# Kernel optimization log

Hardware: AMD Instinct MI355X
Metric: run time of the kernel (lower is better)

The kernel has to match this reference:

```python
import jax, jax.numpy as jnp
import numpy as np

DIM = 768
N_HEADS = 12
HEAD_DIM = DIM // N_HEADS
HIDDEN = int(DIM * 4.0)
B, S = 4, 2048
EPS = 1e-6
SCALE = HEAD_DIM ** -0.5


def layer_norm(x, gamma, beta):
    mu = jnp.mean(x, axis=-1, keepdims=True)
    var = jnp.mean((x - mu) ** 2, axis=-1, keepdims=True)
    return (x - mu) * jax.lax.rsqrt(var + EPS) * gamma + beta


def setup_inputs() -> dict:
    key = jax.random.key(0)
    ks = jax.random.split(key, 8)
    x = jax.random.normal(ks[0], (B, S, DIM), dtype=jnp.float32)
    mask = jax.random.randint(ks[1], (B, 1, S, S), 0, 2, dtype=jnp.int32)
    sd = DIM ** -0.5
    return {
        "x": x,
        "mask": mask,
        "w_qkv": jax.random.normal(ks[2], (DIM, 3 * DIM), dtype=jnp.float32) * sd,
        "b_qkv": jnp.zeros((3 * DIM,), jnp.float32),
        "w_proj": jax.random.normal(ks[3], (DIM, DIM), dtype=jnp.float32) * sd,
        "b_proj": jnp.zeros((DIM,), jnp.float32),
        "g1": jnp.ones((DIM,), jnp.float32),
        "beta1": jnp.zeros((DIM,), jnp.float32),
        "g2": jnp.ones((DIM,), jnp.float32),
        "beta2": jnp.zeros((DIM,), jnp.float32),
        "w1": jax.random.normal(ks[4], (DIM, HIDDEN), dtype=jnp.float32) * sd,
        "b1": jnp.zeros((HIDDEN,), jnp.float32),
        "w2": jax.random.normal(ks[5], (HIDDEN, DIM), dtype=jnp.float32) * (HIDDEN ** -0.5),
        "b2": jnp.zeros((DIM,), jnp.float32),
    }


def reference(x, mask, w_qkv, b_qkv, w_proj, b_proj, g1, beta1, g2, beta2, w1, b1, w2, b2):
    # --- attention branch (pre-LN) ---
    h = layer_norm(x, g1, beta1)
    qkv = h @ w_qkv + b_qkv                              # (B,S,3*DIM)
    qkv = qkv.reshape(B, S, 3, N_HEADS, HEAD_DIM)
    q, k, v = (qkv[:, :, 0], qkv[:, :, 1], qkv[:, :, 2])  # (B,S,H,D)
    # scores: (B,H,S,S) -- materialized like the original
    dp = jnp.einsum("bqhd,bkhd->bhqk", q, k) * SCALE
    dp = jnp.where(mask == 0, jnp.float32(-10000.0), dp)
    attn = jax.nn.softmax(dp, axis=-1)
    wa = jnp.einsum("bhqk,bkhd->bqhd", attn, v).reshape(B, S, DIM)
    x = x + (wa @ w_proj + b_proj)
    # --- MLP branch (pre-LN) ---
    h = layer_norm(x, g2, beta2)
    h = jax.nn.gelu(h @ w1 + b1, approximate=False)
    x = x + (h @ w2 + b2)
    return x
```

## Files before the change

kernel.cpp:

```cpp
#include <hip/hip_runtime.h>
#include <hip/hip_bf16.h>
#include <math.h>

typedef __bf16 bf16;
typedef __bf16 bf16x8 __attribute__((ext_vector_type(8)));
typedef short bf16x4s __attribute__((ext_vector_type(4)));
typedef float f32x4 __attribute__((ext_vector_type(4)));

#define DIM 768
#define NH 12
#define HD 64
#define HID 3072
#define BB 4
#define SS 2048
#define QPRESCALE 0.18033688011112042f

#define MFMA(a, b, c) __builtin_amdgcn_mfma_f32_16x16x32_bf16(a, b, c, 0, 0, 0)
#define MFMA16(a, b, c) \
  __builtin_amdgcn_mfma_f32_16x16x16bf16_1k(a, b, c, 0, 0, 0)

__device__ __forceinline__ void gld16(const void* g, void* l) {
  __builtin_amdgcn_global_load_lds(
      (const __attribute__((address_space(1))) void*)g,
      (__attribute__((address_space(3))) void*)l, 16, 0, 0);
}

__device__ __forceinline__ unsigned pk2(float a, float b) {
  union {
    bf16 h[2];
    unsigned u;
  } t;
  t.h[0] = (bf16)a;
  t.h[1] = (bf16)b;
  return t.u;
}

__global__ __launch_bounds__(256) void castT_all_kernel(
    const float* __restrict__ s0, bf16* __restrict__ d0,
    const float* __restrict__ s1, bf16* __restrict__ d1,
    const float* __restrict__ s2, bf16* __restrict__ d2,
    const float* __restrict__ s3, bf16* __restrict__ d3) {
  __shared__ float tile[32][33];
  int id = blockIdx.x;
  const float* in;
  bf16* out;
  int R, C, loc;
  if (id < 1728) { in = s0; out = d0; R = 768; C = 2304; loc = id; }
  else if (id < 2304) { in = s1; out = d1; R = 768; C = 768; loc = id - 1728; }
  else if (id < 4608) { in = s2; out = d2; R = 768; C = 3072; loc = id - 2304; }
  else { in = s3; out = d3; R = 3072; C = 768; loc = id - 4608; }
  const int cb = C >> 5;
  const int c0 = (loc % cb) * 32, r0 = (loc / cb) * 32;
  const int tx = threadIdx.x & 31, ty = threadIdx.x >> 5;
#pragma unroll
  for (int i = 0; i < 32; i += 8)
    tile[ty + i][tx] = in[(size_t)(r0 + ty + i) * C + c0 + tx];
  __syncthreads();
#pragma unroll
  for (int i = 0; i < 32; i += 8)
    out[(size_t)(c0 + ty + i) * R + r0 + tx] = (bf16)tile[tx][ty + i];
}

__global__ __launch_bounds__(256) void maskbits_kernel(
    const int* __restrict__ mask, unsigned* __restrict__ bits) {
  const int i = blockIdx.x * 256 + threadIdx.x;
  unsigned long long m = __ballot(mask[i] != 0);
  const int lane = threadIdx.x & 63;
  if (lane == 0) bits[i >> 5] = (unsigned)m;
  else if (lane == 32) bits[i >> 5] = (unsigned)(m >> 32);
}

__global__ __launch_bounds__(256) void ln_kernel(
    const float* __restrict__ x, const float* __restrict__ g,
    const float* __restrict__ beta, bf16* __restrict__ out) {
  const int row = blockIdx.x, t = threadIdx.x;
  const float* xr = x + (size_t)row * DIM;
  float v0 = xr[t], v1 = xr[t + 256], v2 = xr[t + 512];
  float s = v0 + v1 + v2;
  float s2 = v0 * v0 + v1 * v1 + v2 * v2;
#pragma unroll
  for (int d = 1; d < 64; d <<= 1) {
    s += __shfl_xor(s, d);
    s2 += __shfl_xor(s2, d);
  }
  __shared__ float red[8];
  const int wv = t >> 6, lane = t & 63;
  if (lane == 0) { red[wv] = s; red[wv + 4] = s2; }
  __syncthreads();
  s = red[0] + red[1] + red[2] + red[3];
  s2 = red[4] + red[5] + red[6] + red[7];
  const float mu = s * (1.0f / DIM);
  const float var = s2 * (1.0f / DIM) - mu * mu;
  const float r = rsqrtf(var + 1e-6f);
  bf16* o = out + (size_t)row * DIM;
  o[t] = (bf16)((v0 - mu) * r * g[t] + beta[t]);
  o[t + 256] = (bf16)((v1 - mu) * r * g[t + 256] + beta[t + 256]);
  o[t + 512] = (bf16)((v2 - mu) * r * g[t + 512] + beta[t + 512]);
}

enum { EPI_QKV = 0, EPI_PROJ = 1, EPI_FFN1 = 2, EPI_FFN2 = 3 };

template <int EPI, int K, int TN>
__global__ __launch_bounds__(256) void gemm_kernel(
    const bf16* __restrict__ A, const bf16* __restrict__ Bt,
    const float* __restrict__ bias, const float* __restrict__ res,
    void* __restrict__ o0, void* __restrict__ o1, void* __restrict__ o2) {
  constexpr int MI = (TN == 128) ? 4 : 2;
  __shared__ bf16 As[128 * 64];
  __shared__ bf16 Bs[TN * 64];
  const int tid = threadIdx.x;
  const int wv = tid >> 6, lane = tid & 63;
  const int quad = lane >> 4, l15 = lane & 15;
  const int lrow = lane >> 3, lcol = lane & 7;
  const int m0 = blockIdx.y * 128, n0 = blockIdx.x * TN;
  const int wm = (TN == 128) ? (wv >> 1) * 64 : wv * 32;
  const int wn = (TN == 128) ? (wv & 1) * 64 : 0;

  f32x4 acc[MI][4] = {};

  const int swz = (lcol ^ lrow) * 8;
  const bf16* Ag = A + (size_t)(m0 + wv * 32 + lrow) * K + swz;
  const bf16* Bg = Bt + (size_t)(n0 + wv * (TN / 4) + lrow) * K + swz;
  bf16* Al = As + (wv * 32) * 64;
  bf16* Bl = Bs + (wv * (TN / 4)) * 64;

  for (int k0 = 0; k0 < K; k0 += 64) {
#pragma unroll
    for (int i = 0; i < 4; i++)
      gld16(Ag + (size_t)(i * 8) * K + k0, Al + i * 8 * 64);
#pragma unroll
    for (int i = 0; i < TN / 32; i++)
      gld16(Bg + (size_t)(i * 8) * K + k0, Bl + i * 8 * 64);
    __syncthreads();
#pragma unroll
    for (int ks = 0; ks < 2; ks++) {
      bf16x8 af[MI], bfr[4];
#pragma unroll
      for (int i = 0; i < MI; i++) {
        const int ra = wm + i * 16 + l15;
        af[i] = *(const bf16x8*)&As[ra * 64 + ((ks * 4 + quad) ^ (ra & 7)) * 8];
      }
#pragma unroll
      for (int i = 0; i < 4; i++) {
        const int rb = wn + i * 16 + l15;
        bfr[i] = *(const bf16x8*)&Bs[rb * 64 + ((ks * 4 + quad) ^ (rb & 7)) * 8];
      }
#pragma unroll
      for (int mi = 0; mi < MI; mi++)
#pragma unroll
        for (int ni = 0; ni < 4; ni++)
          acc[mi][ni] = MFMA(af[mi], bfr[ni], acc[mi][ni]);
    }
    __syncthreads();
  }

#pragma unroll
  for (int mi = 0; mi < MI; mi++) {
#pragma unroll
    for (int ni = 0; ni < 4; ni++) {
      const int n = n0 + wn + ni * 16 + l15;
      const float bv = bias[n];
      const int mb = m0 + wm + mi * 16 + quad * 4;
      float val[4];
#pragma unroll
      for (int r = 0; r < 4; r++) val[r] = acc[mi][ni][r] + bv;
      if (EPI == EPI_QKV) {
        const int which = n / 768;
        const int nn = n - which * 768;
        const int hh = nn >> 6, d = nn & 63;
        const int bb = mb >> 11, s = mb & 2047;
        if (which == 0) {
#pragma unroll
          for (int r = 0; r < 4; r++)
            ((bf16*)o0)[((size_t)(bb * NH + hh) * SS + s + r) * HD + d] =
                (bf16)(val[r] * QPRESCALE);
        } else if (which == 1) {
#pragma unroll
          for (int r = 0; r < 4; r++)
            ((bf16*)o1)[((size_t)(bb * NH + hh) * SS + s + r) * HD + d] =
                (bf16)val[r];
        } else {
          uint2 pv;
          pv.x = pk2(val[0], val[1]);
          pv.y = pk2(val[2], val[3]);
          *(uint2*)&((bf16*)o2)[((size_t)(bb * NH + hh) * HD + d) * SS + s] = pv;
        }
      } else if (EPI == EPI_PROJ) {
#pragma unroll
        for (int r = 0; r < 4; r++)
          ((float*)o0)[(size_t)(mb + r) * DIM + n] =
              res[(size_t)(mb + r) * DIM + n] + val[r];
      } else if (EPI == EPI_FFN1) {
#pragma unroll
        for (int r = 0; r < 4; r++) {
          const float ge =
              0.5f * val[r] * (1.0f + erff(val[r] * 0.70710678118654752f));
          ((bf16*)o0)[(size_t)(mb + r) * HID + n] = (bf16)ge;
        }
      } else {
#pragma unroll
        for (int r = 0; r < 4; r++)
          ((float*)o0)[(size_t)(mb + r) * DIM + n] =
              res[(size_t)(mb + r) * DIM + n] + val[r];
      }
    }
  }
}

__global__ __launch_bounds__(256) void attn_kernel(
    const bf16* __restrict__ q, const bf16* __restrict__ k,
    const bf16* __restrict__ vT, const unsigned* __restrict__ bits,
    bf16* __restrict__ wa) {
  const int b = blockIdx.z, h = blockIdx.y, q0 = blockIdx.x * 64;
  const int tid = threadIdx.x, wv = tid >> 6, lane = tid & 63;
  const int quad = lane >> 4, l15 = lane & 15;
  const int lrow = lane >> 3, lcol = lane & 7;

  __shared__ bf16 Ks[64 * 64];
  __shared__ bf16 Vs[64 * 64];
  __shared__ unsigned lut[32];

  if (tid < 16) {
    lut[2 * tid] =
        ((tid & 1) ? 0xFFFFu : 0u) | ((tid & 2) ? 0xFFFF0000u : 0u);
    lut[2 * tid + 1] =
        ((tid & 4) ? 0xFFFFu : 0u) | ((tid & 8) ? 0xFFFF0000u : 0u);
  }

  const bf16* qbh = q + (size_t)(b * NH + h) * SS * HD;
  const bf16* kbh = k + (size_t)(b * NH + h) * SS * HD;
  const bf16* vbh = vT + (size_t)(b * NH + h) * HD * SS;

  const int sq = q0 + wv * 16 + l15;
  bf16x8 aq[2];
#pragma unroll
  for (int ks = 0; ks < 2; ks++)
    aq[ks] = *(const bf16x8*)&qbh[(size_t)sq * HD + ks * 32 + quad * 8];

  const unsigned long long* mrow =
      (const unsigned long long*)bits + (size_t)(b * SS + sq) * 32;

  f32x4 O[4] = {};
  f32x4 lm = {};
  const short oneb = 0x3F80;
  const bf16x4s onesA = {oneb, oneb, oneb, oneb};
  const int swz = (lcol ^ lrow) * 8;

  for (int s0 = 0; s0 < SS; s0 += 64) {
#pragma unroll
    for (int i = 0; i < 2; i++) {
      const int r = wv * 16 + i * 8 + lrow;
      gld16(&kbh[(size_t)(s0 + r) * HD + swz], &Ks[(wv * 16 + i * 8) * 64]);
      gld16(&vbh[(size_t)r * SS + s0 + swz], &Vs[(wv * 16 + i * 8) * 64]);
    }
    const unsigned long long sh = mrow[s0 >> 6] >> (quad * 4);
    const unsigned lo32 = (unsigned)sh, hi32 = (unsigned)(sh >> 32);
    __syncthreads();

#pragma unroll
    for (int ni = 0; ni < 4; ni++) {
      const int rr = ni * 16 + l15;
      const bf16x8 kf0 =
          *(const bf16x8*)&Ks[rr * 64 + (quad ^ (rr & 7)) * 8];
      const bf16x8 kf1 =
          *(const bf16x8*)&Ks[rr * 64 + ((4 + quad) ^ (rr & 7)) * 8];
      f32x4 a = {};
      a = MFMA(kf0, aq[0], a);
      a = MFMA(kf1, aq[1], a);
      const unsigned nib = (ni == 0)   ? (lo32 & 0xF)
                           : (ni == 1) ? ((lo32 >> 16) & 0xF)
                           : (ni == 2) ? (hi32 & 0xF)
                                       : ((hi32 >> 16) & 0xF);
      const uint2 mw = *(const uint2*)&lut[2 * nib];
      union {
        unsigned u[2];
        bf16x4s v;
      } pp;
      pp.u[0] = pk2(__builtin_amdgcn_exp2f(a[0]),
                    __builtin_amdgcn_exp2f(a[1])) & mw.x;
      pp.u[1] = pk2(__builtin_amdgcn_exp2f(a[2]),
                    __builtin_amdgcn_exp2f(a[3])) & mw.y;
      lm = MFMA16(onesA, pp.v, lm);
#pragma unroll
      for (int nd = 0; nd < 4; nd++) {
        const int row = nd * 16 + l15;
        const int pc = (ni * 2 + (quad >> 1)) ^ (row & 7);
        const bf16x4s vf =
            *(const bf16x4s*)&Vs[row * 64 + pc * 8 + (quad & 1) * 4];
        O[nd] = MFMA16(vf, pp.v, O[nd]);
      }
    }
    __syncthreads();
  }

  const float rln = __builtin_amdgcn_rcpf(lm[0]);
  bf16* dst = wa + (size_t)(b * SS + sq) * DIM + h * HD + quad * 4;
#pragma unroll
  for (int nd = 0; nd < 4; nd++) {
    uint2 pv;
    pv.x = pk2(O[nd][0] * rln, O[nd][1] * rln);
    pv.y = pk2(O[nd][2] * rln, O[nd][3] * rln);
    *(uint2*)&dst[nd * 16] = pv;
  }
}

extern "C" void kernel_launch(void* const* d_in, const int* in_sizes, int n_in,
                              void* d_out, int out_size, void* d_ws,
                              size_t ws_size, hipStream_t stream) {
  const float* x = (const float*)d_in[0];
  const int* mask = (const int*)d_in[1];
  const float* w_qkv = (const float*)d_in[2];
  const float* b_qkv = (const float*)d_in[3];
  const float* w_proj = (const float*)d_in[4];
  const float* b_proj = (const float*)d_in[5];
  const float* g1 = (const float*)d_in[6];
  const float* beta1 = (const float*)d_in[7];
  const float* g2 = (const float*)d_in[8];
  const float* beta2 = (const float*)d_in[9];
  const float* w1 = (const float*)d_in[10];
  const float* b1 = (const float*)d_in[11];
  const float* w2 = (const float*)d_in[12];
  const float* b2 = (const float*)d_in[13];
  float* out = (float*)d_out;

  char* p = (char*)d_ws;
  auto alloc = [&](size_t bytes) {
    char* r = p;
    p += (bytes + 1023) & ~(size_t)1023;
    return r;
  };
  bf16* wqkvT = (bf16*)alloc((size_t)2304 * 768 * 2);
  bf16* wprojT = (bf16*)alloc((size_t)768 * 768 * 2);
  bf16* w1T = (bf16*)alloc((size_t)3072 * 768 * 2);
  bf16* w2T = (bf16*)alloc((size_t)768 * 3072 * 2);
  unsigned* bits = (unsigned*)alloc((size_t)BB * SS * 64 * 4);
  bf16* h = (bf16*)alloc((size_t)8192 * 768 * 2);
  bf16* qb = (bf16*)alloc((size_t)8192 * 768 * 2);
  bf16* kb = (bf16*)alloc((size_t)8192 * 768 * 2);
  bf16* vtb = (bf16*)alloc((size_t)8192 * 768 * 2);
  bf16* wab = (bf16*)alloc((size_t)8192 * 768 * 2);
  float* x2 = (float*)alloc((size_t)8192 * 768 * 4);
  bf16* ffn1 = (bf16*)alloc((size_t)8192 * 3072 * 2);

  castT_all_kernel<<<6912, 256, 0, stream>>>(w_qkv, wqkvT, w_proj, wprojT, w1,
                                             w1T, w2, w2T);
  maskbits_kernel<<<(BB * SS * SS) / 256, 256, 0, stream>>>(mask, bits);
  ln_kernel<<<8192, 256, 0, stream>>>(x, g1, beta1, h);
  gemm_kernel<EPI_QKV, 768, 128>
      <<<dim3(2304 / 128, 8192 / 128), 256, 0, stream>>>(h, wqkvT, b_qkv,
                                                         nullptr, qb, kb, vtb);
  attn_kernel<<<dim3(SS / 64, NH, BB), 256, 0, stream>>>(qb, kb, vtb, bits,
                                                         wab);
  gemm_kernel<EPI_PROJ, 768, 64>
      <<<dim3(768 / 64, 8192 / 128), 256, 0, stream>>>(wab, wprojT, b_proj, x,
                                                       x2, nullptr, nullptr);
  ln_kernel<<<8192, 256, 0, stream>>>(x2, g2, beta2, h);
  gemm_kernel<EPI_FFN1, 768, 128>
      <<<dim3(3072 / 128, 8192 / 128), 256, 0, stream>>>(h, w1T, b1, nullptr,
                                                         ffn1, nullptr,
                                                         nullptr);
  gemm_kernel<EPI_FFN2, 3072, 64>
      <<<dim3(768 / 64, 8192 / 128), 256, 0, stream>>>(ffn1, w2T, b2, x2, out,
                                                       nullptr, nullptr);
}
```

Baseline: 495.2 us.

## Double-buffer LDS tiles in GEMM and attention kernels to overlap loads

Both the GEMM kernel and the attention kernel now use two LDS buffers. The next K/V or A/B tile is issued via global_load_lds while the current tile is consumed, and the mask word is prefetched one iteration ahead. This keeps one barrier per iteration instead of two and aims to hide global-load latency behind MFMA work. The cost is doubled shared memory, which may reduce occupancy. Correctness relies on the compiler's vmcnt wait before the barrier, since the async LDS loads are only fenced by __syncthreads.

```diff
diff --git a/kernel.cpp b/kernel.cpp
--- a/kernel.cpp
+++ b/kernel.cpp
@@ -106,8 +106,9 @@
     const float* __restrict__ bias, const float* __restrict__ res,
     void* __restrict__ o0, void* __restrict__ o1, void* __restrict__ o2) {
   constexpr int MI = (TN == 128) ? 4 : 2;
-  __shared__ bf16 As[128 * 64];
-  __shared__ bf16 Bs[TN * 64];
+  constexpr int NIT = K / 64;
+  __shared__ bf16 As[2][128 * 64];
+  __shared__ bf16 Bs[2][TN * 64];
   const int tid = threadIdx.x;
   const int wv = tid >> 6, lane = tid & 63;
   const int quad = lane >> 4, l15 = lane & 15;
@@ -121,29 +122,37 @@
   const int swz = (lcol ^ lrow) * 8;
   const bf16* Ag = A + (size_t)(m0 + wv * 32 + lrow) * K + swz;
   const bf16* Bg = Bt + (size_t)(n0 + wv * (TN / 4) + lrow) * K + swz;
-  bf16* Al = As + (wv * 32) * 64;
-  bf16* Bl = Bs + (wv * (TN / 4)) * 64;
-
-  for (int k0 = 0; k0 < K; k0 += 64) {
+
+  auto stage = [&](int buf, int k0) {
 #pragma unroll
     for (int i = 0; i < 4; i++)
-      gld16(Ag + (size_t)(i * 8) * K + k0, Al + i * 8 * 64);
+      gld16(Ag + (size_t)(i * 8) * K + k0, &As[buf][(wv * 32 + i * 8) * 64]);
 #pragma unroll
     for (int i = 0; i < TN / 32; i++)
-      gld16(Bg + (size_t)(i * 8) * K + k0, Bl + i * 8 * 64);
+      gld16(Bg + (size_t)(i * 8) * K + k0,
+            &Bs[buf][(wv * (TN / 4) + i * 8) * 64]);
+  };
+
+  stage(0, 0);
+
+  for (int it = 0; it < NIT; ++it) {
     __syncthreads();
+    if (it + 1 < NIT) stage((it + 1) & 1, (it + 1) * 64);
+    const bf16* Ab = As[it & 1];
+    const bf16* Bb = Bs[it & 1];
 #pragma unroll
     for (int ks = 0; ks < 2; ks++) {
       bf16x8 af[MI], bfr[4];
 #pragma unroll
       for (int i = 0; i < MI; i++) {
         const int ra = wm + i * 16 + l15;
-        af[i] = *(const bf16x8*)&As[ra * 64 + ((ks * 4 + quad) ^ (ra & 7)) * 8];
+        af[i] = *(const bf16x8*)&Ab[ra * 64 + ((ks * 4 + quad) ^ (ra & 7)) * 8];
       }
 #pragma unroll
       for (int i = 0; i < 4; i++) {
         const int rb = wn + i * 16 + l15;
-        bfr[i] = *(const bf16x8*)&Bs[rb * 64 + ((ks * 4 + quad) ^ (rb & 7)) * 8];
+        bfr[i] =
+            *(const bf16x8*)&Bb[rb * 64 + ((ks * 4 + quad) ^ (rb & 7)) * 8];
       }
 #pragma unroll
       for (int mi = 0; mi < MI; mi++)
@@ -151,7 +160,6 @@
         for (int ni = 0; ni < 4; ni++)
           acc[mi][ni] = MFMA(af[mi], bfr[ni], acc[mi][ni]);
     }
-    __syncthreads();
   }
 
 #pragma unroll
@@ -216,8 +224,8 @@
   const int quad = lane >> 4, l15 = lane & 15;
   const int lrow = lane >> 3, lcol = lane & 7;
 
-  __shared__ bf16 Ks[64 * 64];
-  __shared__ bf16 Vs[64 * 64];
+  __shared__ bf16 Ks[2][64 * 64];
+  __shared__ bf16 Vs[2][64 * 64];
   __shared__ unsigned lut[32];
 
   if (tid < 16) {
@@ -246,24 +254,38 @@
   const bf16x4s onesA = {oneb, oneb, oneb, oneb};
   const int swz = (lcol ^ lrow) * 8;
 
-  for (int s0 = 0; s0 < SS; s0 += 64) {
+  auto stageKV = [&](int buf, int s0) {
 #pragma unroll
     for (int i = 0; i < 2; i++) {
       const int r = wv * 16 + i * 8 + lrow;
-      gld16(&kbh[(size_t)(s0 + r) * HD + swz], &Ks[(wv * 16 + i * 8) * 64]);
-      gld16(&vbh[(size_t)r * SS + s0 + swz], &Vs[(wv * 16 + i * 8) * 64]);
-    }
-    const unsigned long long sh = mrow[s0 >> 6] >> (quad * 4);
+      gld16(&kbh[(size_t)(s0 + r) * HD + swz],
+            &Ks[buf][(wv * 16 + i * 8) * 64]);
+      gld16(&vbh[(size_t)r * SS + s0 + swz],
+            &Vs[buf][(wv * 16 + i * 8) * 64]);
+    }
+  };
+
+  stageKV(0, 0);
+  unsigned long long mw = mrow[0];
+
+  for (int t = 0; t < SS / 64; ++t) {
+    __syncthreads();
+    unsigned long long mwn = 0;
+    if (t + 1 < SS / 64) {
+      stageKV((t + 1) & 1, (t + 1) * 64);
+      mwn = mrow[t + 1];
+    }
+    const bf16* Kc = Ks[t & 1];
+    const bf16* Vc = Vs[t & 1];
+    const unsigned long long sh = mw >> (quad * 4);
     const unsigned lo32 = (unsigned)sh, hi32 = (unsigned)(sh >> 32);
-    __syncthreads();
 
 #pragma unroll
     for (int ni = 0; ni < 4; ni++) {
       const int rr = ni * 16 + l15;
-      const bf16x8 kf0 =
-          *(const bf16x8*)&Ks[rr * 64 + (quad ^ (rr & 7)) * 8];
+      const bf16x8 kf0 = *(const bf16x8*)&Kc[rr * 64 + (quad ^ (rr & 7)) * 8];
       const bf16x8 kf1 =
-          *(const bf16x8*)&Ks[rr * 64 + ((4 + quad) ^ (rr & 7)) * 8];
+          *(const bf16x8*)&Kc[rr * 64 + ((4 + quad) ^ (rr & 7)) * 8];
       f32x4 a = {};
       a = MFMA(kf0, aq[0], a);
       a = MFMA(kf1, aq[1], a);
@@ -271,26 +293,26 @@
                            : (ni == 1) ? ((lo32 >> 16) & 0xF)
                            : (ni == 2) ? (hi32 & 0xF)
                                        : ((hi32 >> 16) & 0xF);
-      const uint2 mw = *(const uint2*)&lut[2 * nib];
+      const uint2 mwrd = *(const uint2*)&lut[2 * nib];
       union {
         unsigned u[2];
         bf16x4s v;
       } pp;
       pp.u[0] = pk2(__builtin_amdgcn_exp2f(a[0]),
-                    __builtin_amdgcn_exp2f(a[1])) & mw.x;
+                    __builtin_amdgcn_exp2f(a[1])) & mwrd.x;
       pp.u[1] = pk2(__builtin_amdgcn_exp2f(a[2]),
-                    __builtin_amdgcn_exp2f(a[3])) & mw.y;
+                    __builtin_amdgcn_exp2f(a[3])) & mwrd.y;
       lm = MFMA16(onesA, pp.v, lm);
 #pragma unroll
       for (int nd = 0; nd < 4; nd++) {
         const int row = nd * 16 + l15;
         const int pc = (ni * 2 + (quad >> 1)) ^ (row & 7);
         const bf16x4s vf =
-            *(const bf16x4s*)&Vs[row * 64 + pc * 8 + (quad & 1) * 4];
+            *(const bf16x4s*)&Vc[row * 64 + pc * 8 + (quad & 1) * 4];
         O[nd] = MFMA16(vf, pp.v, O[nd]);
       }
     }
-    __syncthreads();
+    mw = mwn;
   }
 
   const float rln = __builtin_amdgcn_rcpf(lm[0]);
```

Result: slower. 528.8 us (+6.8%).

## Process two 16-row query tiles per wave in attention to reuse K/V tiles

Applied to the files above, without the earlier changes.

Each attention block now covers 128 query rows instead of 64, and each wave handles two 16-row query sub-tiles that share the same K and V fragments read from LDS. This halves global K/V loads per query and the LDS fragment reads per MFMA, and halves the grid size. In exchange, per-thread register use roughly doubles for accumulators, and there are fewer blocks (768) to fill the GPU, which may reduce occupancy.

```diff
diff --git a/kernel.cpp b/kernel.cpp
--- a/kernel.cpp
+++ b/kernel.cpp
@@ -211,7 +211,7 @@
     const bf16* __restrict__ q, const bf16* __restrict__ k,
     const bf16* __restrict__ vT, const unsigned* __restrict__ bits,
     bf16* __restrict__ wa) {
-  const int b = blockIdx.z, h = blockIdx.y, q0 = blockIdx.x * 64;
+  const int b = blockIdx.z, h = blockIdx.y, q0 = blockIdx.x * 128;
   const int tid = threadIdx.x, wv = tid >> 6, lane = tid & 63;
   const int quad = lane >> 4, l15 = lane & 15;
   const int lrow = lane >> 3, lcol = lane & 7;
@@ -231,76 +231,101 @@
   const bf16* kbh = k + (size_t)(b * NH + h) * SS * HD;
   const bf16* vbh = vT + (size_t)(b * NH + h) * HD * SS;
 
-  const int sq = q0 + wv * 16 + l15;
-  bf16x8 aq[2];
-#pragma unroll
-  for (int ks = 0; ks < 2; ks++)
-    aq[ks] = *(const bf16x8*)&qbh[(size_t)sq * HD + ks * 32 + quad * 8];
-
-  const unsigned long long* mrow =
-      (const unsigned long long*)bits + (size_t)(b * SS + sq) * 32;
-
-  f32x4 O[4] = {};
-  f32x4 lm = {};
+  bf16x8 aq[2][2];
+#pragma unroll
+  for (int mi = 0; mi < 2; mi++)
+#pragma unroll
+    for (int ks = 0; ks < 2; ks++) {
+      const int s = q0 + wv * 32 + mi * 16 + l15;
+      aq[mi][ks] = *(const bf16x8*)&qbh[(size_t)s * HD + ks * 32 + quad * 8];
+    }
+
+  const unsigned long long* mrow[2];
+#pragma unroll
+  for (int mi = 0; mi < 2; mi++)
+    mrow[mi] = (const unsigned long long*)bits +
+               (size_t)(b * SS + q0 + wv * 32 + mi * 16 + l15) * 32;
+
+  f32x4 O[2][4] = {};
+  f32x4 lm[2] = {};
   const short oneb = 0x3F80;
   const bf16x4s onesA = {oneb, oneb, oneb, oneb};
   const int swz = (lcol ^ lrow) * 8;
 
-  for (int s0 = 0; s0 < SS; s0 += 64) {
+  for (int t = 0; t < SS / 64; ++t) {
+    const int s0 = t * 64;
 #pragma unroll
     for (int i = 0; i < 2; i++) {
       const int r = wv * 16 + i * 8 + lrow;
       gld16(&kbh[(size_t)(s0 + r) * HD + swz], &Ks[(wv * 16 + i * 8) * 64]);
       gld16(&vbh[(size_t)r * SS + s0 + swz], &Vs[(wv * 16 + i * 8) * 64]);
     }
-    const unsigned long long sh = mrow[s0 >> 6] >> (quad * 4);
-    const unsigned lo32 = (unsigned)sh, hi32 = (unsigned)(sh >> 32);
+    const unsigned long long sh0 = mrow[0][t] >> (quad * 4);
+    const unsigned long long sh1 = mrow[1][t] >> (quad * 4);
+    const unsigned lo0 = (unsigned)sh0, hi0 = (unsigned)(sh0 >> 32);
+    const unsigned lo1 = (unsigned)sh1, hi1 = (unsigned)(sh1 >> 32);
     __syncthreads();
 
 #pragma unroll
     for (int ni = 0; ni < 4; ni++) {
       const int rr = ni * 16 + l15;
-      const bf16x8 kf0 =
-          *(const bf16x8*)&Ks[rr * 64 + (quad ^ (rr & 7)) * 8];
+      const bf16x8 kf0 = *(const bf16x8*)&Ks[rr * 64 + (quad ^ (rr & 7)) * 8];
       const bf16x8 kf1 =
           *(const bf16x8*)&Ks[rr * 64 + ((4 + quad) ^ (rr & 7)) * 8];
-      f32x4 a = {};
-      a = MFMA(kf0, aq[0], a);
-      a = MFMA(kf1, aq[1], a);
-      const unsigned nib = (ni == 0)   ? (lo32 & 0xF)
-                           : (ni == 1) ? ((lo32 >> 16) & 0xF)
-                           : (ni == 2) ? (hi32 & 0xF)
-                                       : ((hi32 >> 16) & 0xF);
-      const uint2 mw = *(const uint2*)&lut[2 * nib];
+      f32x4 a0 = {}, a1 = {};
+      a0 = MFMA(kf0, aq[0][0], a0);
+      a0 = MFMA(kf1, aq[0][1], a0);
+      a1 = MFMA(kf0, aq[1][0], a1);
+      a1 = MFMA(kf1, aq[1][1], a1);
+      const unsigned nib0 = (ni == 0)   ? (lo0 & 0xF)
+                            : (ni == 1) ? ((lo0 >> 16) & 0xF)
+                            : (ni == 2) ? (hi0 & 0xF)
+                                        : ((hi0 >> 16) & 0xF);
+      const unsigned nib1 = (ni == 0)   ? (lo1 & 0xF)
+                            : (ni == 1) ? ((lo1 >> 16) & 0xF)
+                            : (ni == 2) ? (hi1 & 0xF)
+                                        : ((hi1 >> 16) & 0xF);
+      const uint2 mw0 = *(const uint2*)&lut[2 * nib0];
+      const uint2 mw1 = *(const uint2*)&lut[2 * nib1];
       union {
         unsigned u[2];
         bf16x4s v;
-      } pp;
-      pp.u[0] = pk2(__builtin_amdgcn_exp2f(a[0]),
-                    __builtin_amdgcn_exp2f(a[1])) & mw.x;
-      pp.u[1] = pk2(__builtin_amdgcn_exp2f(a[2]),
-                    __builtin_amdgcn_exp2f(a[3])) & mw.y;
-      lm = MFMA16(onesA, pp.v, lm);
+      } p0, p1;
+      p0.u[0] = pk2(__builtin_amdgcn_exp2f(a0[0]),
+                    __builtin_amdgcn_exp2f(a0[1])) & mw0.x;
+      p0.u[1] = pk2(__builtin_amdgcn_exp2f(a0[2]),
+                    __builtin_amdgcn_exp2f(a0[3])) & mw0.y;
+      p1.u[0] = pk2(__builtin_amdgcn_exp2f(a1[0]),
+                    __builtin_amdgcn_exp2f(a1[1])) & mw1.x;
+      p1.u[1] = pk2(__builtin_amdgcn_exp2f(a1[2]),
+                    __builtin_amdgcn_exp2f(a1[3])) & mw1.y;
+      lm[0] = MFMA16(onesA, p0.v, lm[0]);
+      lm[1] = MFMA16(onesA, p1.v, lm[1]);
 #pragma unroll
       for (int nd = 0; nd < 4; nd++) {
         const int row = nd * 16 + l15;
         const int pc = (ni * 2 + (quad >> 1)) ^ (row & 7);
         const bf16x4s vf =
             *(const bf16x4s*)&Vs[row * 64 + pc * 8 + (quad & 1) * 4];
-        O[nd] = MFMA16(vf, pp.v, O[nd]);
+        O[0][nd] = MFMA16(vf, p0.v, O[0][nd]);
+        O[1][nd] = MFMA16(vf, p1.v, O[1][nd]);
       }
     }
     __syncthreads();
   }
 
-  const float rln = __builtin_amdgcn_rcpf(lm[0]);
-  bf16* dst = wa + (size_t)(b * SS + sq) * DIM + h * HD + quad * 4;
-#pragma unroll
-  for (int nd = 0; nd < 4; nd++) {
-    uint2 pv;
-    pv.x = pk2(O[nd][0] * rln, O[nd][1] * rln);
-    pv.y = pk2(O[nd][2] * rln, O[nd][3] * rln);
-    *(uint2*)&dst[nd * 16] = pv;
+#pragma unroll
+  for (int mi = 0; mi < 2; mi++) {
+    const float rln = __builtin_amdgcn_rcpf(lm[mi][0]);
+    const int sq = q0 + wv * 32 + mi * 16 + l15;
+    bf16* dst = wa + (size_t)(b * SS + sq) * DIM + h * HD + quad * 4;
+#pragma unroll
+    for (int nd = 0; nd < 4; nd++) {
+      uint2 pv;
+      pv.x = pk2(O[mi][nd][0] * rln, O[mi][nd][1] * rln);
+      pv.y = pk2(O[mi][nd][2] * rln, O[mi][nd][3] * rln);
+      *(uint2*)&dst[nd * 16] = pv;
+    }
   }
 }
 
@@ -349,8 +374,8 @@
   gemm_kernel<EPI_QKV, 768, 128>
       <<<dim3(2304 / 128, 8192 / 128), 256, 0, stream>>>(h, wqkvT, b_qkv,
                                                          nullptr, qb, kb, vtb);
-  attn_kernel<<<dim3(SS / 64, NH, BB), 256, 0, stream>>>(qb, kb, vtb, bits,
-                                                         wab);
+  attn_kernel<<<dim3(SS / 128, NH, BB), 256, 0, stream>>>(qb, kb, vtb, bits,
+                                                          wab);
   gemm_kernel<EPI_PROJ, 768, 64>
       <<<dim3(768 / 64, 8192 / 128), 256, 0, stream>>>(wab, wprojT, b_proj, x,
                                                        x2, nullptr, nullptr);
```

New measurement: 505.1 us. +2.0%, slower.
